# Kernel optimization log

Measured on AMD Instinct MI355X. Metric: run time of the kernel, lower is better.

Reference implementation:

```python
import jax, jax.numpy as jnp
import numpy as np

NEG_SLOPE = 0.2  # PyG GATConv default LeakyReLU slope

N_NODES = 100000
N_EDGES = 1600000
IN_CH = 256
HEADS = 4
OUT_CH = 64


def setup_inputs() -> dict:
    key = jax.random.key(0)
    k1, k2, k3, k4, k5 = jax.random.split(key, 5)
    x = jax.random.normal(k1, (N_NODES, IN_CH), dtype=jnp.float32)
    edge_index = jax.random.randint(k2, (2, N_EDGES), 0, N_NODES, dtype=jnp.int64)
    # Glorot-ish scaled params
    W = jax.random.normal(k3, (IN_CH, HEADS * OUT_CH), dtype=jnp.float32) / np.sqrt(IN_CH)
    att_src = jax.random.normal(k4, (HEADS, OUT_CH), dtype=jnp.float32) / np.sqrt(OUT_CH)
    att_dst = jax.random.normal(k5, (HEADS, OUT_CH), dtype=jnp.float32) / np.sqrt(OUT_CH)
    bias = jnp.zeros((HEADS * OUT_CH,), dtype=jnp.float32)
    return {"graph_node_features": x, "edge_index": edge_index,
            "W": W, "att_src": att_src, "att_dst": att_dst, "bias": bias}


def reference(graph_node_features, edge_index, W, att_src, att_dst, bias):
    x = graph_node_features
    N = x.shape[0]
    H, C = att_src.shape

    # Linear projection, per-head view: [N, H, C]
    x_lin = (x @ W).reshape(N, H, C)

    # Per-node attention logits: [N, H]
    a_src = jnp.einsum('nhc,hc->nh', x_lin, att_src)
    a_dst = jnp.einsum('nhc,hc->nh', x_lin, att_dst)

    # Add self-loops (PyG add_self_loops=True default)
    loop = jnp.arange(N, dtype=edge_index.dtype)
    src = jnp.concatenate([edge_index[0], loop])
    dst = jnp.concatenate([edge_index[1], loop])

    # Edge attention logits with LeakyReLU: [E, H]
    alpha = jax.nn.leaky_relu(a_src[src] + a_dst[dst], NEG_SLOPE)

    # Segment softmax over incoming edges of each destination node
    amax = jax.ops.segment_max(alpha, dst, num_segments=N)  # [N, H]
    amax = jnp.where(jnp.isfinite(amax), amax, 0.0)
    ex = jnp.exp(alpha - amax[dst])
    denom = jax.ops.segment_sum(ex, dst, num_segments=N)  # [N, H]
    alpha_n = ex / (denom[dst] + 1e-16)

    # Weighted scatter-add of source features: [N, H, C]
    msg = x_lin[src] * alpha_n[:, :, None]
    out = jax.ops.segment_sum(msg, dst, num_segments=N)

    # Concat heads + bias (concat=True default)
    return out.reshape(N, H * C) + bias
```

## Files before the change

### kernel.cpp

```cpp
#include <hip/hip_runtime.h>

#define IN_CH  256
#define HCC    256
#define HEADS  4
#define OUTC   64
#define NEG_SLOPE 0.2f

#define NBUK   512
#define NBLK   64
#define CAP    192
#define ECAP   4608
#define SRC_BITS 17
#define SRC_MASK 0x1FFFF

using short8v = __attribute__((ext_vector_type(8))) short;
using f32x4   = __attribute__((ext_vector_type(4))) float;

__device__ __forceinline__ unsigned short f2bf(float f) {
    unsigned u = __float_as_uint(f);
    unsigned r = (u + 0x7fffu + ((u >> 16) & 1u)) >> 16;
    return (unsigned short)r;
}
__device__ __forceinline__ float bf2f(unsigned short b) {
    return __uint_as_float((unsigned)b << 16);
}
__device__ __forceinline__ int buk_of(int dst, unsigned M) {
    unsigned s = (unsigned)(((unsigned long long)(unsigned)dst * M) >> 32);
    return (s >= NBUK) ? (NBUK - 1) : (int)s;
}
__device__ __forceinline__ void gload_lds16(const unsigned short* g,
                                            unsigned short* lds) {
    __builtin_amdgcn_global_load_lds(
        (const __attribute__((address_space(1))) unsigned*)g,
        (__attribute__((address_space(3))) unsigned*)lds, 16, 0, 0);
}

__global__ void k_wt(const float* __restrict__ W,
                     unsigned short* __restrict__ WT) {
    int n = blockIdx.x;
    int k = threadIdx.x;
    WT[n * IN_CH + k] = f2bf(W[(size_t)k * HCC + n]);
}

__global__ __launch_bounds__(256) void k_gemm_part(
    const float* __restrict__ X, const unsigned short* __restrict__ WT,
    const float* __restrict__ ASRC, const float* __restrict__ ADST,
    unsigned short* __restrict__ XLB, float* __restrict__ a_s,
    float* __restrict__ a_d, int N,
    const int* __restrict__ ei, unsigned* __restrict__ pedges,
    int* __restrict__ cnt2d, int E, unsigned M, int rng) {
    __shared__ unsigned short Ats[64][40];
    __shared__ __align__(16) unsigned short Bs[256 * 32];
    __shared__ int cur[NBUK];

    if (blockIdx.x < NBLK) {
        int bid = blockIdx.x;
        int t = threadIdx.x;
        for (int k = t; k < NBUK; k += 256) cur[k] = 0;
        __syncthreads();
        int chunk = (E + NBLK - 1) / NBLK;
        int e0 = bid * chunk;
        int e1 = e0 + chunk;
        if (e1 > E) e1 = E;
        for (int i = e0 + t; i < e1; i += 256) {
            int src = ei[i];
            int dst = ei[E + i];
            int s = buk_of(dst, M);
            int pos = atomicAdd(&cur[s], 1);
            if (pos < CAP)
                pedges[((size_t)s * NBLK + bid) * CAP + pos] =
                    ((unsigned)(dst - s * rng) << SRC_BITS) | (unsigned)src;
        }
        __syncthreads();
        for (int k = t; k < NBUK; k += 256) {
            int c = cur[k];
            cnt2d[k * NBLK + bid] = (c > CAP) ? CAP : c;
        }
        return;
    }

    const int tid = threadIdx.x;
    const int lane = tid & 63;
    const int wid = tid >> 6;
    const int m0 = (blockIdx.x - NBLK) * 64;
    const int r16 = lane & 15;
    const int g = lane >> 4;
    const int cs = (lane & 3) ^ ((lane >> 3) & 3);

    f32x4 acc[4][4];
    const f32x4 z = {0.f, 0.f, 0.f, 0.f};
#pragma unroll
    for (int m = 0; m < 4; ++m)
#pragma unroll
        for (int n = 0; n < 4; ++n) acc[m][n] = z;

    for (int kb = 0; kb < IN_CH; kb += 32) {
#pragma unroll
        for (int i = 0; i < 4; ++i) {
            int r0 = wid * 64 + i * 16;
            int row = r0 + (lane >> 2);
            gload_lds16(WT + (size_t)row * IN_CH + kb + cs * 8,
                        &Bs[r0 * 32]);
        }
#pragma unroll
        for (int it = 0; it < 2; ++it) {
            int v = tid + 256 * it;
            int row = v >> 3;
            int c4 = (v & 7) << 2;
            int gr = m0 + row;
            float4 av = make_float4(0.f, 0.f, 0.f, 0.f);
            if (gr < N) av = *(const float4*)(X + (size_t)gr * IN_CH + kb + c4);
            ushort4 ab;
            ab.x = f2bf(av.x); ab.y = f2bf(av.y);
            ab.z = f2bf(av.z); ab.w = f2bf(av.w);
            *(ushort4*)&Ats[row][c4] = ab;
        }
        __syncthreads();
        short8v af[4], bf[4];
#pragma unroll
        for (int m = 0; m < 4; ++m)
            af[m] = *(const short8v*)&Ats[m * 16 + r16][g * 8];
#pragma unroll
        for (int n = 0; n < 4; ++n) {
            int row = wid * 64 + n * 16 + r16;
            int ck = g ^ ((r16 >> 1) & 3);
            bf[n] = *(const short8v*)&Bs[row * 32 + ck * 8];
        }
#pragma unroll
        for (int m = 0; m < 4; ++m)
#pragma unroll
            for (int n = 0; n < 4; ++n)
                acc[m][n] = __builtin_amdgcn_mfma_f32_16x16x32_bf16(
                    af[m], bf[n], acc[m][n], 0, 0, 0);
        __syncthreads();
    }

    const int h = wid;
    float asc[4], adc[4];
#pragma unroll
    for (int n = 0; n < 4; ++n) {
        asc[n] = ASRC[h * OUTC + n * 16 + r16];
        adc[n] = ADST[h * OUTC + n * 16 + r16];
    }

#pragma unroll
    for (int m = 0; m < 4; ++m) {
#pragma unroll
        for (int j = 0; j < 4; ++j) {
            int row = m0 + m * 16 + g * 4 + j;
            float ds = 0.f, dd = 0.f;
#pragma unroll
            for (int n = 0; n < 4; ++n) {
                ds = fmaf(acc[m][n][j], asc[n], ds);
                dd = fmaf(acc[m][n][j], adc[n], dd);
            }
#pragma unroll
            for (int o = 1; o < 16; o <<= 1) {
                ds += __shfl_xor(ds, o);
                dd += __shfl_xor(dd, o);
            }
            if (row < N && r16 == 0) {
                a_s[(size_t)row * HEADS + h] = ds;
                a_d[(size_t)row * HEADS + h] = dd;
            }
        }
    }

    unsigned short* Cs = Bs;
#pragma unroll
    for (int p = 0; p < 2; ++p) {
        if (p) __syncthreads();
#pragma unroll
        for (int mm = 0; mm < 2; ++mm) {
            int m = p * 2 + mm;
#pragma unroll
            for (int j = 0; j < 4; ++j) {
                int lr = mm * 16 + g * 4 + j;
                int sx = lr & 7;
#pragma unroll
                for (int n = 0; n < 4; ++n) {
                    int col = wid * 64 + n * 16 + r16;
                    int sub = col >> 2, wi = col & 3;
                    Cs[lr * 256 + ((sub ^ sx) << 2) + wi] = f2bf(acc[m][n][j]);
                }
            }
        }
        __syncthreads();
#pragma unroll
        for (int it = 0; it < 8; ++it) {
            int lr = wid + it * 4;
            int gr = m0 + p * 32 + lr;
            if (gr < N) {
                int sx = lr & 7;
                uint2 v = *(const uint2*)&Cs[lr * 256 + ((lane ^ sx) << 2)];
                *(uint2*)(XLB + (size_t)gr * HCC + lane * 4) = v;
            }
        }
    }
}

__global__ __launch_bounds__(1024) void k_bagg(
    const int* __restrict__ cnt2d, const unsigned* __restrict__ pedges,
    const float* __restrict__ a_s, const float* __restrict__ a_d,
    const unsigned short* __restrict__ XLB, const float* __restrict__ BIAS,
    float* __restrict__ OUT, int N, int rng) {
    __shared__ int cntL[256];
    __shared__ int scanL[256];
    __shared__ int rowL[256];
    __shared__ int fillL[256];
    __shared__ int segc[NBLK];
    __shared__ int eidL[ECAP];

    int k = blockIdx.x;
    int t = threadIdx.x;
    int lo = k * rng;
    if (lo >= N) return;
    int nloc = N - lo;
    if (nloc > rng) nloc = rng;

    if (t < NBLK) segc[t] = cnt2d[k * NBLK + t];
    if (t < 256) cntL[t] = 0;
    __syncthreads();

    int b = t >> 4;
    int sub = t & 15;
    const unsigned* seg = pedges + ((size_t)k * NBLK + b) * CAP;
    int cb = segc[b];
    for (int i = sub; i < cb; i += 16)
        atomicAdd(&cntL[seg[i] >> SRC_BITS], 1);
    __syncthreads();

    int own = (t < 256 && t < nloc) ? cntL[t] + 1 : 0;
    if (t < 256) scanL[t] = own;
    __syncthreads();
    for (int off = 1; off < 256; off <<= 1) {
        int x = (t < 256 && t >= off) ? scanL[t - off] : 0;
        __syncthreads();
        if (t < 256) scanL[t] += x;
        __syncthreads();
    }
    if (t < 256) {
        int excl = scanL[t] - own;
        rowL[t] = excl;
        if (t < nloc) {
            eidL[excl] = lo + t;
            fillL[t] = excl + 1;
        }
    }
    __syncthreads();

    for (int i = sub; i < cb; i += 16) {
        unsigned pk = seg[i];
        int dl = (int)(pk >> SRC_BITS);
        int pos = atomicAdd(&fillL[dl], 1);
        if (pos < ECAP) eidL[pos] = (int)(pk & SRC_MASK);
    }
    __syncthreads();

    int wv = t >> 6;
    int lane = t & 63;
    int h = lane >> 4;
    float4 bv = *(const float4*)(BIAS + lane * 4);
    for (int nl = wv; nl < nloc; nl += 16) {
        int n = lo + nl;
        int s0 = rowL[nl];
        int s1 = scanL[nl];
        float adn = a_d[(size_t)n * HEADS + h];
        float s = 0.f;
        float acc0 = 0.f, acc1 = 0.f, acc2 = 0.f, acc3 = 0.f;

        int e = s0;
        for (; e + 8 <= s1; e += 8) {
            int idx[8];
#pragma unroll
            for (int j = 0; j < 8; ++j) idx[j] = eidL[e + j];
            float l[8];
#pragma unroll
            for (int j = 0; j < 8; ++j)
                l[j] = a_s[(size_t)idx[j] * HEADS + h] + adn;
            ushort4 xv[8];
#pragma unroll
            for (int j = 0; j < 8; ++j)
                xv[j] = *(const ushort4*)(XLB + (size_t)idx[j] * HCC + lane * 4);
#pragma unroll
            for (int j = 0; j < 8; ++j) {
                float lj = fmaxf(l[j], NEG_SLOPE * l[j]);
                float p = __expf(lj);
                s += p;
                acc0 = fmaf(p, bf2f(xv[j].x), acc0);
                acc1 = fmaf(p, bf2f(xv[j].y), acc1);
                acc2 = fmaf(p, bf2f(xv[j].z), acc2);
                acc3 = fmaf(p, bf2f(xv[j].w), acc3);
            }
        }
        for (; e + 4 <= s1; e += 4) {
            int idx[4];
#pragma unroll
            for (int j = 0; j < 4; ++j) idx[j] = eidL[e + j];
            float l[4];
#pragma unroll
            for (int j = 0; j < 4; ++j)
                l[j] = a_s[(size_t)idx[j] * HEADS + h] + adn;
            ushort4 xv[4];
#pragma unroll
            for (int j = 0; j < 4; ++j)
                xv[j] = *(const ushort4*)(XLB + (size_t)idx[j] * HCC + lane * 4);
#pragma unroll
            for (int j = 0; j < 4; ++j) {
                float lj = fmaxf(l[j], NEG_SLOPE * l[j]);
                float p = __expf(lj);
                s += p;
                acc0 = fmaf(p, bf2f(xv[j].x), acc0);
                acc1 = fmaf(p, bf2f(xv[j].y), acc1);
                acc2 = fmaf(p, bf2f(xv[j].z), acc2);
                acc3 = fmaf(p, bf2f(xv[j].w), acc3);
            }
        }
        for (; e < s1; ++e) {
            int src = eidL[e];
            float l = a_s[(size_t)src * HEADS + h] + adn;
            l = fmaxf(l, NEG_SLOPE * l);
            float p = __expf(l);
            ushort4 xv = *(const ushort4*)(XLB + (size_t)src * HCC + lane * 4);
            s += p;
            acc0 = fmaf(p, bf2f(xv.x), acc0);
            acc1 = fmaf(p, bf2f(xv.y), acc1);
            acc2 = fmaf(p, bf2f(xv.z), acc2);
            acc3 = fmaf(p, bf2f(xv.w), acc3);
        }

        float inv = 1.f / (s + 1e-16f);
        f32x4 o;
        o[0] = acc0 * inv + bv.x;
        o[1] = acc1 * inv + bv.y;
        o[2] = acc2 * inv + bv.z;
        o[3] = acc3 * inv + bv.w;
        __builtin_nontemporal_store(
            o, (f32x4*)(OUT + (size_t)n * HCC + lane * 4));
    }
}

extern "C" void kernel_launch(void* const* d_in, const int* in_sizes, int n_in,
                              void* d_out, int out_size, void* d_ws,
                              size_t ws_size, hipStream_t stream) {
    const float* X = (const float*)d_in[0];
    const int* EI = (const int*)d_in[1];
    const float* W = (const float*)d_in[2];
    const float* ASRC = (const float*)d_in[3];
    const float* ADST = (const float*)d_in[4];
    const float* BIAS = (const float*)d_in[5];
    float* OUT = (float*)d_out;

    const int N = in_sizes[0] / IN_CH;
    const int E = in_sizes[1] / 2;
    const int rng = (N + NBUK - 1) / NBUK;
    const unsigned M = (unsigned)(((1ULL << 32) + rng - 1) / (unsigned)rng);

    char* w = (char*)d_ws;
    auto align = [](size_t x) { return (x + 255) & ~(size_t)255; };
    size_t o = 0;
    unsigned short* xlb = (unsigned short*)(w + o); o += align((size_t)N * HCC * 2);
    unsigned short* wt = (unsigned short*)(w + o);  o += align((size_t)IN_CH * HCC * 2);
    float* a_s = (float*)(w + o); o += align((size_t)N * HEADS * 4);
    float* a_d = (float*)(w + o); o += align((size_t)N * HEADS * 4);
    unsigned* pedges = (unsigned*)(w + o); o += align((size_t)NBUK * NBLK * CAP * 4);
    int* cnt2d = (int*)(w + o);   o += align((size_t)NBUK * NBLK * 4);

    k_wt<<<HCC, IN_CH, 0, stream>>>(W, wt);

    int ngemm = (N + 63) / 64;
    k_gemm_part<<<NBLK + ngemm, 256, 0, stream>>>(X, wt, ASRC, ADST, xlb,
                                                  a_s, a_d, N, EI, pedges,
                                                  cnt2d, E, M, rng);

    k_bagg<<<NBUK, 1024, 0, stream>>>(cnt2d, pedges, a_s, a_d, xlb, BIAS,
                                      OUT, N, rng);
}
```

Baseline: 231.6 us.

## Precompute per-edge attention weights in LDS during bucketing, unroll gather by 16

During the edge bucketing phase, each edge's four per-head exp(leaky_relu) weights are computed once and stored as bf16 in a new shared array alongside the source index. The aggregation loop then reads weights from LDS instead of doing a dependent global load of a_s followed by an exp, and the main loop is unrolled to 16 edges for more outstanding feature gathers. This removes redundant per-lane exp and a_s loads (previously each of 64 lanes recomputed them) at the cost of extra LDS (about 36KB), bf16 rounding of the weights, and more register pressure.

```diff
diff --git a/kernel.cpp b/kernel.cpp
--- a/kernel.cpp
+++ b/kernel.cpp
@@ -210,6 +210,7 @@
     __shared__ int fillL[256];
     __shared__ int segc[NBLK];
     __shared__ int eidL[ECAP];
+    __shared__ ushort4 pwL[ECAP];
 
     int k = blockIdx.x;
     int t = threadIdx.x;
@@ -243,7 +244,18 @@
         int excl = scanL[t] - own;
         rowL[t] = excl;
         if (t < nloc) {
-            eidL[excl] = lo + t;
+            int n = lo + t;
+            float4 as4 = *(const float4*)(a_s + (size_t)n * HEADS);
+            float4 ad4 = *(const float4*)(a_d + (size_t)n * HEADS);
+            float l0 = as4.x + ad4.x, l1 = as4.y + ad4.y;
+            float l2 = as4.z + ad4.z, l3 = as4.w + ad4.w;
+            l0 = fmaxf(l0, NEG_SLOPE * l0); l1 = fmaxf(l1, NEG_SLOPE * l1);
+            l2 = fmaxf(l2, NEG_SLOPE * l2); l3 = fmaxf(l3, NEG_SLOPE * l3);
+            ushort4 pw;
+            pw.x = f2bf(__expf(l0)); pw.y = f2bf(__expf(l1));
+            pw.z = f2bf(__expf(l2)); pw.w = f2bf(__expf(l3));
+            eidL[excl] = n;
+            pwL[excl] = pw;
             fillL[t] = excl + 1;
         }
     }
@@ -252,8 +264,21 @@
     for (int i = sub; i < cb; i += 16) {
         unsigned pk = seg[i];
         int dl = (int)(pk >> SRC_BITS);
+        int src = (int)(pk & SRC_MASK);
+        float4 as4 = *(const float4*)(a_s + (size_t)src * HEADS);
+        float4 ad4 = *(const float4*)(a_d + (size_t)(lo + dl) * HEADS);
+        float l0 = as4.x + ad4.x, l1 = as4.y + ad4.y;
+        float l2 = as4.z + ad4.z, l3 = as4.w + ad4.w;
+        l0 = fmaxf(l0, NEG_SLOPE * l0); l1 = fmaxf(l1, NEG_SLOPE * l1);
+        l2 = fmaxf(l2, NEG_SLOPE * l2); l3 = fmaxf(l3, NEG_SLOPE * l3);
+        ushort4 pw;
+        pw.x = f2bf(__expf(l0)); pw.y = f2bf(__expf(l1));
+        pw.z = f2bf(__expf(l2)); pw.w = f2bf(__expf(l3));
         int pos = atomicAdd(&fillL[dl], 1);
-        if (pos < ECAP) eidL[pos] = (int)(pk & SRC_MASK);
+        if (pos < ECAP) {
+            eidL[pos] = src;
+            pwL[pos] = pw;
+        }
     }
     __syncthreads();
 
@@ -265,62 +290,55 @@
         int n = lo + nl;
         int s0 = rowL[nl];
         int s1 = scanL[nl];
-        float adn = a_d[(size_t)n * HEADS + h];
         float s = 0.f;
         float acc0 = 0.f, acc1 = 0.f, acc2 = 0.f, acc3 = 0.f;
 
         int e = s0;
-        for (; e + 8 <= s1; e += 8) {
-            int idx[8];
-#pragma unroll
-            for (int j = 0; j < 8; ++j) idx[j] = eidL[e + j];
-            float l[8];
-#pragma unroll
-            for (int j = 0; j < 8; ++j)
-                l[j] = a_s[(size_t)idx[j] * HEADS + h] + adn;
-            ushort4 xv[8];
-#pragma unroll
-            for (int j = 0; j < 8; ++j)
+        for (; e + 16 <= s1; e += 16) {
+            int idx[16];
+            float p[16];
+#pragma unroll
+            for (int j = 0; j < 16; ++j) {
+                idx[j] = eidL[e + j];
+                p[j] = bf2f(((const unsigned short*)&pwL[e + j])[h]);
+            }
+            ushort4 xv[16];
+#pragma unroll
+            for (int j = 0; j < 16; ++j)
                 xv[j] = *(const ushort4*)(XLB + (size_t)idx[j] * HCC + lane * 4);
 #pragma unroll
-            for (int j = 0; j < 8; ++j) {
-                float lj = fmaxf(l[j], NEG_SLOPE * l[j]);
-                float p = __expf(lj);
-                s += p;
-                acc0 = fmaf(p, bf2f(xv[j].x), acc0);
-                acc1 = fmaf(p, bf2f(xv[j].y), acc1);
-                acc2 = fmaf(p, bf2f(xv[j].z), acc2);
-                acc3 = fmaf(p, bf2f(xv[j].w), acc3);
+            for (int j = 0; j < 16; ++j) {
+                s += p[j];
+                acc0 = fmaf(p[j], bf2f(xv[j].x), acc0);
+                acc1 = fmaf(p[j], bf2f(xv[j].y), acc1);
+                acc2 = fmaf(p[j], bf2f(xv[j].z), acc2);
+                acc3 = fmaf(p[j], bf2f(xv[j].w), acc3);
             }
         }
         for (; e + 4 <= s1; e += 4) {
             int idx[4];
-#pragma unroll
-            for (int j = 0; j < 4; ++j) idx[j] = eidL[e + j];
-            float l[4];
-#pragma unroll
-            for (int j = 0; j < 4; ++j)
-                l[j] = a_s[(size_t)idx[j] * HEADS + h] + adn;
+            float p[4];
+#pragma unroll
+            for (int j = 0; j < 4; ++j) {
+                idx[j] = eidL[e + j];
+                p[j] = bf2f(((const unsigned short*)&pwL[e + j])[h]);
+            }
             ushort4 xv[4];
 #pragma unroll
             for (int j = 0; j < 4; ++j)
                 xv[j] = *(const ushort4*)(XLB + (size_t)idx[j] * HCC + lane * 4);
 #pragma unroll
             for (int j = 0; j < 4; ++j) {
-                float lj = fmaxf(l[j], NEG_SLOPE * l[j]);
-                float p = __expf(lj);
-                s += p;
-                acc0 = fmaf(p, bf2f(xv[j].x), acc0);
-                acc1 = fmaf(p, bf2f(xv[j].y), acc1);
-                acc2 = fmaf(p, bf2f(xv[j].z), acc2);
-                acc3 = fmaf(p, bf2f(xv[j].w), acc3);
+                s += p[j];
+                acc0 = fmaf(p[j], bf2f(xv[j].x), acc0);
+                acc1 = fmaf(p[j], bf2f(xv[j].y), acc1);
+                acc2 = fmaf(p[j], bf2f(xv[j].z), acc2);
+                acc3 = fmaf(p[j], bf2f(xv[j].w), acc3);
             }
         }
         for (; e < s1; ++e) {
             int src = eidL[e];
-            float l = a_s[(size_t)src * HEADS + h] + adn;
-            l = fmaxf(l, NEG_SLOPE * l);
-            float p = __expf(l);
+            float p = bf2f(((const unsigned short*)&pwL[e])[h]);
             ushort4 xv = *(const ushort4*)(XLB + (size_t)src * HCC + lane * 4);
             s += p;
             acc0 = fmaf(p, bf2f(xv.x), acc0);
```

Result: faster. 222.7 us (median of 2 runs) (-3.8%).
